# Kernel tuning notes

Measured on AMD Instinct MI355X. Metric: run time of the kernel, lower is better.

Reference implementation:

```python
import jax, jax.numpy as jnp
import numpy as np
from jax import lax

TOP_K = 4
ROUTED_SCALING = 1.0
RENORMALIZE = True


def setup_inputs() -> dict:
    key = jax.random.key(0)
    ks = jax.random.split(key, 9)
    H, I, E = 2048, 1024, 16
    s = 0.02
    return {
        "hidden_states": jax.random.normal(ks[0], (2, 1024, H), jnp.float32),
        "gate_w": jax.random.normal(ks[1], (E, H), jnp.float32) * s,
        "expert_bias": jax.random.normal(ks[2], (E,), jnp.float32) * s,
        "w_gate": jax.random.normal(ks[3], (E, I, H), jnp.float32) * s,
        "w_up": jax.random.normal(ks[4], (E, I, H), jnp.float32) * s,
        "w_down": jax.random.normal(ks[5], (E, H, I), jnp.float32) * s,
        "sw_gate": jax.random.normal(ks[6], (I, H), jnp.float32) * s,
        "sw_up": jax.random.normal(ks[7], (I, H), jnp.float32) * s,
        "sw_down": jax.random.normal(ks[8], (H, I), jnp.float32) * s,
    }


def _swiglu_ffn(x, wg, wu, wd):
    # SiluAndMul(gate_up) -> down_proj
    return (jax.nn.silu(x @ wg.T) * (x @ wu.T)) @ wd.T


def reference(hidden_states, gate_w, expert_bias, w_gate, w_up, w_down,
              sw_gate, sw_up, sw_down):
    orig_shape = hidden_states.shape
    H = orig_shape[-1]
    x = hidden_states.reshape(-1, H)            # [T, H]
    T = x.shape[0]

    # --- sigmoid gating with score-correction bias (bias affects selection only) ---
    logits = x.astype(jnp.float32) @ gate_w.T    # [T, E] fp32 router
    scores = jax.nn.sigmoid(logits)
    _, topk_idx = lax.top_k(scores + expert_bias[None, :], TOP_K)   # [T, K]
    topk_w = jnp.take_along_axis(scores, topk_idx, axis=-1)         # raw scores
    if RENORMALIZE:
        topk_w = topk_w / jnp.sum(topk_w, axis=-1, keepdims=True)
    topk_w = topk_w * ROUTED_SCALING

    # scatter top-k weights into dense [T, E] combine matrix
    E = gate_w.shape[0]
    combine = jnp.zeros((T, E), dtype=x.dtype).at[
        jnp.arange(T)[:, None], topk_idx].set(topk_w.astype(x.dtype))

    # --- routed experts: scan over experts, weighted accumulate ---
    def step(acc, ws):
        wg, wu, wd, cw = ws                     # cw: [T] combine weights
        return acc + cw[:, None] * _swiglu_ffn(x, wg, wu, wd), None

    routed, _ = lax.scan(step, jnp.zeros_like(x),
                         (w_gate, w_up, w_down, combine.T))

    # --- shared expert ---
    shared = _swiglu_ffn(x, sw_gate, sw_up, sw_down)

    return (routed + shared).reshape(orig_shape)
```

## Files before the change

kernel.cpp:

```cpp
#include <hip/hip_runtime.h>
#include <hip/hip_bf16.h>
#include <cstdint>

#define TK 2048
#define HD 2048
#define ID 1024
#define NE 16
#define NG 17
#define TOPK 4
#define SLOTS (TK*TOPK)
#define ROWS_ALL (SLOTS+TK)
#define IH (ID*HD)
#define MAXT 64

typedef __attribute__((ext_vector_type(4))) float f32x4;
typedef __attribute__((ext_vector_type(16))) float f32x16;
typedef __attribute__((ext_vector_type(8))) short s16x8;
typedef unsigned short u16;
typedef unsigned long long u64;

__device__ __forceinline__ u16 f2bf(float f){
  union { float f; uint32_t u; } v; v.f = f;
  uint32_t r = v.u + 0x7fffu + ((v.u >> 16) & 1u);
  return (u16)(r >> 16);
}

#define GLD16(g, l) __builtin_amdgcn_global_load_lds( \
    (const __attribute__((address_space(1))) void*)(g), \
    (__attribute__((address_space(3))) void*)(l), 16, 0, 0)

__device__ __forceinline__ const s16x8* fragp(const u16* b, int row, int off){
  return (const s16x8*)((const char*)b + row*128 + (off ^ ((row&7)<<4)));
}

#define MFMA32(a,b,c) __builtin_amdgcn_mfma_f32_32x32x16_bf16((a),(b),(c),0,0,0)

__global__ void k_prep(const float* __restrict__ x, u16* __restrict__ xb,
                       u64* __restrict__ maskbits, int* __restrict__ tokcnt){
  int gi = blockIdx.x*blockDim.x + threadIdx.x;
  int st = gridDim.x*blockDim.x;
  if (gi < NE*32) maskbits[gi] = 0ull;
  if (gi < TK) tokcnt[gi] = 0;
  for (int i=gi; i<TK*HD/4; i+=st){
    float4 f = ((const float4*)x)[i];
    ushort4 o; o.x=f2bf(f.x); o.y=f2bf(f.y); o.z=f2bf(f.z); o.w=f2bf(f.w);
    ((ushort4*)xb)[i] = o;
  }
}

__global__ void k_cvtw(const float* __restrict__ wg, const float* __restrict__ wu,
                       const float* __restrict__ wd, const float* __restrict__ swg,
                       const float* __restrict__ swu, const float* __restrict__ swd,
                       u16* __restrict__ wgu, u16* __restrict__ wdb){
  const size_t ngu = (size_t)NG*2048*(HD/4);
  const size_t nd  = (size_t)NG*2048*(ID/4);
  for (size_t i = (size_t)blockIdx.x*blockDim.x + threadIdx.x; i < ngu + nd;
       i += (size_t)gridDim.x*blockDim.x){
    const float4* src; ushort4* dst;
    if (i < ngu){
      int g   = (int)(i / (2048*(size_t)(HD/4)));
      int rem = (int)(i % (2048*(size_t)(HD/4)));
      int J   = rem / (HD/4);
      int kv  = rem % (HD/4);
      int rp  = (J>>6)*32 + (J&31);
      const float* s;
      if (g < NE) s = ((J&32) ? wu : wg) + (size_t)g*IH + (size_t)rp*HD;
      else        s = ((J&32) ? swu : swg) + (size_t)rp*HD;
      src = (const float4*)s + kv;
      dst = (ushort4*)(wgu + (size_t)g*2048*HD + (size_t)J*HD) + kv;
    } else {
      size_t j = i - ngu;
      int g   = (int)(j / (2048*(size_t)(ID/4)));
      int rem = (int)(j % (2048*(size_t)(ID/4)));
      int J   = rem / (ID/4);
      int kv  = rem % (ID/4);
      const float* s = (g < NE) ? (wd + (size_t)g*IH + (size_t)J*ID)
                                : (swd + (size_t)J*ID);
      src = (const float4*)s + kv;
      dst = (ushort4*)(wdb + (size_t)g*2048*ID + (size_t)J*ID) + kv;
    }
    float4 f = *src;
    ushort4 o; o.x=f2bf(f.x); o.y=f2bf(f.y); o.z=f2bf(f.z); o.w=f2bf(f.w);
    *dst = o;
  }
}

__global__ __launch_bounds__(256) void k_logits(const float* __restrict__ x,
                                                const float* __restrict__ gw,
                                                const float* __restrict__ bias,
                                                float* __restrict__ wdense,
                                                u64* __restrict__ maskbits){
  int t = blockIdx.x, tid = threadIdx.x;
  int lane = tid & 63, wv = tid >> 6;
  const float* xr = x + (size_t)t*HD;
  float acc[NE];
  #pragma unroll
  for (int e=0;e<NE;e++) acc[e]=0.f;
  for (int k=tid;k<HD;k+=256){
    float xv = xr[k];
    #pragma unroll
    for (int e=0;e<NE;e++) acc[e] += xv * gw[e*HD + k];
  }
  __shared__ float red[NE][4];
  #pragma unroll
  for (int e=0;e<NE;e++){
    float v = acc[e];
    #pragma unroll
    for (int off=32;off>0;off>>=1) v += __shfl_down(v, off, 64);
    if (lane==0) red[e][wv] = v;
  }
  __syncthreads();
  if (tid == 0){
    float sc[NE], bs[NE];
    #pragma unroll
    for (int e=0;e<NE;e++){
      float l = red[e][0]+red[e][1]+red[e][2]+red[e][3];
      float s = 1.f/(1.f+expf(-l));
      sc[e]=s; bs[e]=s+bias[e];
    }
    int idx[TOPK]; float wsum=0.f; unsigned used=0;
    for (int k=0;k<TOPK;k++){
      int best=0; float bv=-1e30f;
      for (int e=0;e<NE;e++) if (!((used>>e)&1u) && bs[e] > bv){ bv=bs[e]; best=e; }
      used |= 1u<<best; idx[k]=best; wsum += sc[best];
    }
    float inv = 1.f/wsum;
    for (int k=0;k<TOPK;k++){
      int e = idx[k];
      wdense[t*NE + e] = sc[e]*inv;
      atomicOr(&maskbits[e*32 + (t>>6)], 1ull << (t&63));
    }
  }
}

__global__ void k_scan(const u64* __restrict__ maskbits, int* __restrict__ counts,
                       int* __restrict__ offsets, int* __restrict__ wordpfx,
                       int* __restrict__ tiles){
  int acc = 0;
  for (int e=0;e<NE;e++){
    int c = 0;
    for (int w=0;w<32;w++){ wordpfx[e*32+w] = c; c += __popcll(maskbits[e*32+w]); }
    counts[e] = c;
  }
  for (int e=0;e<NE;e++){ offsets[e] = acc; acc += counts[e]; }
  offsets[NE] = acc;
  counts[NE] = TK;
  int nt = 0;
  for (int g=0; g<NG; g++){
    int c = counts[g];
    for (int mt=0; mt*256 < c && nt < MAXT; mt++) tiles[nt++] = (g<<8) | mt;
  }
  for (; nt<MAXT; nt++) tiles[nt] = -1;
}

__global__ void k_scatter(const u64* __restrict__ maskbits, const int* __restrict__ offsets,
                          const int* __restrict__ wordpfx, const float* __restrict__ wdense,
                          int* __restrict__ rowtok, float* __restrict__ roww,
                          int* __restrict__ tokcnt, int* __restrict__ tok4){
  int t = blockIdx.x*blockDim.x + threadIdx.x;
  int e = blockIdx.y;
  if (t >= TK) return;
  if (e == NE){ rowtok[offsets[NE]+t] = t; roww[offsets[NE]+t] = 1.f; return; }
  u64 w = maskbits[e*32 + (t>>6)];
  if ((w >> (t&63)) & 1ull){
    int pos = offsets[e] + wordpfx[e*32 + (t>>6)] + __popcll(w & ((1ull << (t&63)) - 1ull));
    rowtok[pos] = t; roww[pos] = wdense[t*NE + e];
    int r = atomicAdd(&tokcnt[t], 1);
    tok4[t*TOPK + r] = pos;
  }
}

__global__ __launch_bounds__(512, 2) void k_gemm1b(
    const u16* __restrict__ xb, const u16* __restrict__ wgu,
    const int* __restrict__ counts, const int* __restrict__ offsets,
    const int* __restrict__ rowtok, const float* __restrict__ roww,
    const int* __restrict__ tiles, u16* __restrict__ P)
{
  int te = tiles[blockIdx.y];
  if (te < 0) return;
  int g = te >> 8, mt = te & 255;
  int cnt = counts[g];
  int x = blockIdx.x;
  int base = offsets[g];
  const u16* B0 = wgu + (size_t)g*2048*HD + (size_t)(x*256)*HD;

  __shared__ u16 lsA[2][256*64];
  __shared__ u16 lsB[2][256*64];

  int tid = threadIdx.x, lane = tid & 63, wv = tid >> 6;
  int wm = (wv>>2)*128, wc = wv & 3;
  int rl = lane & 31, hi = lane >> 5;

  f32x16 acc[4][2] = {};

  const u16 *aSrc[4], *bSrc[4];
  #pragma unroll
  for (int i=0;i<4;i++){
    int c = i*512 + tid, r = c>>3, cb = c&7;
    int m = mt*256 + r; if (m >= cnt) m = cnt-1;
    int tok = rowtok[base + m];
    aSrc[i] = xb + (size_t)tok*HD + ((cb ^ (r&7))<<3);
    bSrc[i] = B0 + (size_t)r*HD + ((cb ^ (r&7))<<3);
  }

  #pragma unroll
  for (int i=0;i<4;i++) GLD16(aSrc[i], &lsA[0][(i*512 + wv*64)*8]);
  #pragma unroll
  for (int i=0;i<4;i++) GLD16(bSrc[i], &lsB[0][(i*512 + wv*64)*8]);

  const int ntile = HD/64;
  for (int t=0; t<ntile; ++t){
    int cur = t & 1, nxt = cur ^ 1;
    if (t+1 < ntile){
      int k1 = (t+1)*64;
      #pragma unroll
      for (int i=0;i<4;i++) GLD16(aSrc[i]+k1, &lsA[nxt][(i*512 + wv*64)*8]);
      #pragma unroll
      for (int i=0;i<4;i++) GLD16(bSrc[i]+k1, &lsB[nxt][(i*512 + wv*64)*8]);
      asm volatile("s_waitcnt vmcnt(8)" ::: "memory");
    } else {
      asm volatile("s_waitcnt vmcnt(0)" ::: "memory");
    }
    __builtin_amdgcn_s_barrier();
    const u16* A = lsA[cur]; const u16* B = lsB[cur];
    __builtin_amdgcn_s_setprio(1);
    #pragma unroll
    for (int s=0; s<4; ++s){
      int off = s*32 + hi*16;
      s16x8 af[4], bf[2];
      #pragma unroll
      for (int mi=0;mi<4;mi++) af[mi] = *fragp(A, wm + mi*32 + rl, off);
      bf[0] = *fragp(B, wc*64 + rl, off);
      bf[1] = *fragp(B, wc*64 + 32 + rl, off);
      #pragma unroll
      for (int mi=0;mi<4;mi++){
        acc[mi][0] = MFMA32(af[mi], bf[0], acc[mi][0]);
        acc[mi][1] = MFMA32(af[mi], bf[1], acc[mi][1]);
      }
    }
    __builtin_amdgcn_s_setprio(0);
    asm volatile("s_waitcnt lgkmcnt(0)" ::: "memory");
    __builtin_amdgcn_s_barrier();
  }
  int pcol = x*128 + wc*32 + rl;
  #pragma unroll
  for (int mi=0;mi<4;mi++){
    #pragma unroll
    for (int r=0;r<16;r++){
      int rowb = wm + mi*32 + (r&3) + 8*(r>>2) + 4*hi;
      int m = mt*256 + rowb;
      if (m < cnt){
        int slot = base + m;
        float wgt = roww[slot];
        float gv = acc[mi][0][r], uv = acc[mi][1][r];
        float pv = gv/(1.f+expf(-gv))*uv*wgt;
        P[(size_t)slot*ID + pcol] = f2bf(pv);
      }
    }
  }
}

__global__ __launch_bounds__(512, 2) void k_gemm2b(
    const u16* __restrict__ P, const u16* __restrict__ wdb,
    const int* __restrict__ counts, const int* __restrict__ offsets,
    const int* __restrict__ tiles, u16* __restrict__ R)
{
  int te = tiles[blockIdx.y];
  if (te < 0) return;
  int g = te >> 8, mt = te & 255;
  int cnt = counts[g];
  int base = offsets[g];
  int x = blockIdx.x;
  const u16* B0 = wdb + (size_t)g*2048*ID + (size_t)(x*256)*ID;

  __shared__ u16 lsA[2][256*64];
  __shared__ u16 lsB[2][256*64];

  int tid = threadIdx.x, lane = tid & 63, wv = tid >> 6;
  int wm = (wv>>2)*128, wc = wv & 3;
  int rl = lane & 31, hi = lane >> 5;
  f32x16 acc[4][2] = {};

  const u16 *aSrc[4], *bSrc[4];
  #pragma unroll
  for (int i=0;i<4;i++){
    int c = i*512 + tid, r = c>>3, cb = c&7;
    int m = mt*256 + r; if (m >= cnt) m = cnt-1;
    aSrc[i] = P + (size_t)(base + m)*ID + ((cb ^ (r&7))<<3);
    bSrc[i] = B0 + (size_t)r*ID + ((cb ^ (r&7))<<3);
  }

  #pragma unroll
  for (int i=0;i<4;i++) GLD16(aSrc[i], &lsA[0][(i*512 + wv*64)*8]);
  #pragma unroll
  for (int i=0;i<4;i++) GLD16(bSrc[i], &lsB[0][(i*512 + wv*64)*8]);

  const int ntile = ID/64;
  for (int t=0; t<ntile; ++t){
    int cur = t & 1, nxt = cur ^ 1;
    if (t+1 < ntile){
      int k1 = (t+1)*64;
      #pragma unroll
      for (int i=0;i<4;i++) GLD16(aSrc[i]+k1, &lsA[nxt][(i*512 + wv*64)*8]);
      #pragma unroll
      for (int i=0;i<4;i++) GLD16(bSrc[i]+k1, &lsB[nxt][(i*512 + wv*64)*8]);
      asm volatile("s_waitcnt vmcnt(8)" ::: "memory");
    } else {
      asm volatile("s_waitcnt vmcnt(0)" ::: "memory");
    }
    __builtin_amdgcn_s_barrier();
    const u16* A = lsA[cur]; const u16* B = lsB[cur];
    __builtin_amdgcn_s_setprio(1);
    #pragma unroll
    for (int s=0; s<4; ++s){
      int off = s*32 + hi*16;
      s16x8 af[4], bf[2];
      #pragma unroll
      for (int mi=0;mi<4;mi++) af[mi] = *fragp(A, wm + mi*32 + rl, off);
      bf[0] = *fragp(B, wc*64 + rl, off);
      bf[1] = *fragp(B, wc*64 + 32 + rl, off);
      #pragma unroll
      for (int mi=0;mi<4;mi++){
        acc[mi][0] = MFMA32(af[mi], bf[0], acc[mi][0]);
        acc[mi][1] = MFMA32(af[mi], bf[1], acc[mi][1]);
      }
    }
    __builtin_amdgcn_s_setprio(0);
    asm volatile("s_waitcnt lgkmcnt(0)" ::: "memory");
    __builtin_amdgcn_s_barrier();
  }
  #pragma unroll
  for (int mi=0;mi<4;mi++){
    #pragma unroll
    for (int r=0;r<16;r++){
      int rowb = wm + mi*32 + (r&3) + 8*(r>>2) + 4*hi;
      int m = mt*256 + rowb;
      if (m < cnt){
        int slot = base + m;
        u16* rrow = R + (size_t)slot*HD + x*256 + wc*64 + rl;
        rrow[0]  = f2bf(acc[mi][0][r]);
        rrow[32] = f2bf(acc[mi][1][r]);
      }
    }
  }
}

__global__ __launch_bounds__(256) void k_reduce(const u16* __restrict__ R,
                                                const int* __restrict__ tok4,
                                                float* __restrict__ out){
  int t = blockIdx.x;
  int c0 = threadIdx.x * 8;
  int s0 = tok4[t*TOPK+0], s1 = tok4[t*TOPK+1], s2 = tok4[t*TOPK+2], s3 = tok4[t*TOPK+3];
  const ushort4* p0 = (const ushort4*)(R + (size_t)s0*HD + c0);
  const ushort4* p1 = (const ushort4*)(R + (size_t)s1*HD + c0);
  const ushort4* p2 = (const ushort4*)(R + (size_t)s2*HD + c0);
  const ushort4* p3 = (const ushort4*)(R + (size_t)s3*HD + c0);
  const ushort4* ps = (const ushort4*)(R + (size_t)(SLOTS + t)*HD + c0);
  float* o = out + (size_t)t*HD + c0;
  #pragma unroll
  for (int h=0; h<2; h++){
    ushort4 a = p0[h], b = p1[h], c = p2[h], d = p3[h], e = ps[h];
    #pragma unroll
    for (int j=0;j<4;j++){
      u16 ua = ((const u16*)&a)[j], ub = ((const u16*)&b)[j];
      u16 uc = ((const u16*)&c)[j], ud = ((const u16*)&d)[j], ue = ((const u16*)&e)[j];
      union { uint32_t u; float f; } w;
      float v;
      w.u = (uint32_t)ua<<16; v  = w.f;
      w.u = (uint32_t)ub<<16; v += w.f;
      w.u = (uint32_t)uc<<16; v += w.f;
      w.u = (uint32_t)ud<<16; v += w.f;
      w.u = (uint32_t)ue<<16; v += w.f;
      o[h*4 + j] = v;
    }
  }
}


extern "C" void kernel_launch(void* const* d_in, const int* in_sizes, int n_in,
                              void* d_out, int out_size, void* d_ws, size_t ws_size,
                              hipStream_t stream){
  (void)in_sizes; (void)n_in; (void)ws_size; (void)out_size;
  const float* x       = (const float*)d_in[0];
  const float* gate_w  = (const float*)d_in[1];
  const float* ebias   = (const float*)d_in[2];
  const float* w_gate  = (const float*)d_in[3];
  const float* w_up    = (const float*)d_in[4];
  const float* w_down  = (const float*)d_in[5];
  const float* sw_gate = (const float*)d_in[6];
  const float* sw_up   = (const float*)d_in[7];
  const float* sw_down = (const float*)d_in[8];
  float* out = (float*)d_out;

  char* p = (char*)d_ws;
  auto alloc = [&](size_t bytes)->char*{ char* r = p; p += (bytes + 255) & ~(size_t)255; return r; };
  u16*   xb       = (u16*)  alloc((size_t)TK*HD*2);
  u16*   P        = (u16*)  alloc((size_t)ROWS_ALL*ID*2);
  float* wdense   = (float*)alloc((size_t)TK*NE*4);
  u64*   maskbits = (u64*)  alloc((size_t)NE*32*8);
  int*   wordpfx  = (int*)  alloc((size_t)NE*32*4);
  int*   counts   = (int*)  alloc(64);
  int*   offsets  = (int*)  alloc(64);
  int*   tiles    = (int*)  alloc(MAXT*4);
  int*   rowtok   = (int*)  alloc((size_t)ROWS_ALL*4);
  float* roww     = (float*)alloc((size_t)ROWS_ALL*4);
  int*   tokcnt   = (int*)  alloc((size_t)TK*4);
  int*   tok4     = (int*)  alloc((size_t)TK*TOPK*4);
  u16* wgu = (u16*)alloc((size_t)NG*2048*HD*2);
  u16* wdb = (u16*)alloc((size_t)NG*2048*ID*2);
  u16* R = wgu;

  k_prep<<<2048, 256, 0, stream>>>(x, xb, maskbits, tokcnt);
  k_cvtw<<<2048, 256, 0, stream>>>(w_gate, w_up, w_down, sw_gate, sw_up, sw_down,
                                   wgu, wdb);
  k_logits<<<TK, 256, 0, stream>>>(x, gate_w, ebias, wdense, maskbits);
  k_scan<<<1, 1, 0, stream>>>(maskbits, counts, offsets, wordpfx, tiles);
  k_scatter<<<dim3(TK/256, NG), 256, 0, stream>>>(maskbits, offsets, wordpfx, wdense,
                                                  rowtok, roww, tokcnt, tok4);

  dim3 g1(ID/128, MAXT);
  k_gemm1b<<<g1, 512, 0, stream>>>(xb, wgu, counts, offsets, rowtok, roww, tiles, P);
  dim3 g2(HD/256, MAXT);
  k_gemm2b<<<g2, 512, 0, stream>>>(P, wdb, counts, offsets, tiles, R);
  k_reduce<<<TK, 256, 0, stream>>>(R, tok4, out);
}
```

Baseline: 422.8 us.

## Restructure expert GEMMs into 16x16x32 MFMA with split-K interleaved staging

Both grouped expert GEMM kernels now use the 16x16x32 bf16 MFMA instead of 32x32x16. Each 64-wide K tile is split into two 32-wide halves held in separate LDS sub-buffers, with a 4-wide XOR swizzle. Each K step is broken into four compute phases that issue the next tile's A/B half-loads between MFMA bursts, guarded by finer vmcnt waits. The goal is to overlap global-to-LDS traffic with matrix math more evenly instead of issuing all prefetches at once. In exchange there are roughly four times as many barriers per K step and more fragment reads, and the epilogue mapping is rewritten to match the new accumulator layout.

```diff
diff --git a/kernel.cpp b/kernel.cpp
--- a/kernel.cpp
+++ b/kernel.cpp
@@ -14,7 +14,6 @@
 #define MAXT 64
 
 typedef __attribute__((ext_vector_type(4))) float f32x4;
-typedef __attribute__((ext_vector_type(16))) float f32x16;
 typedef __attribute__((ext_vector_type(8))) short s16x8;
 typedef unsigned short u16;
 typedef unsigned long long u64;
@@ -29,11 +28,7 @@
     (const __attribute__((address_space(1))) void*)(g), \
     (__attribute__((address_space(3))) void*)(l), 16, 0, 0)
 
-__device__ __forceinline__ const s16x8* fragp(const u16* b, int row, int off){
-  return (const s16x8*)((const char*)b + row*128 + (off ^ ((row&7)<<4)));
-}
-
-#define MFMA32(a,b,c) __builtin_amdgcn_mfma_f32_32x32x16_bf16((a),(b),(c),0,0,0)
+#define MFMA16(a,b,c) __builtin_amdgcn_mfma_f32_16x16x32_bf16((a),(b),(c),0,0,0)
 
 __global__ void k_prep(const float* __restrict__ x, u16* __restrict__ xb,
                        u64* __restrict__ maskbits, int* __restrict__ tokcnt){
@@ -184,77 +179,136 @@
   int base = offsets[g];
   const u16* B0 = wgu + (size_t)g*2048*HD + (size_t)(x*256)*HD;
 
-  __shared__ u16 lsA[2][256*64];
-  __shared__ u16 lsB[2][256*64];
+  __shared__ u16 lsA[2][2][256*32];
+  __shared__ u16 lsB[2][2][256*32];
 
   int tid = threadIdx.x, lane = tid & 63, wv = tid >> 6;
-  int wm = (wv>>2)*128, wc = wv & 3;
-  int rl = lane & 31, hi = lane >> 5;
-
-  f32x16 acc[4][2] = {};
-
-  const u16 *aSrc[4], *bSrc[4];
-  #pragma unroll
-  for (int i=0;i<4;i++){
-    int c = i*512 + tid, r = c>>3, cb = c&7;
+  int wm = (wv>>2)*128, wc = wv & 3, wn = wc*64;
+  int rl = lane & 15, hi = lane >> 4;
+
+  f32x4 acc[8][4] = {};
+
+  const u16 *aS[2], *bS[2];
+  #pragma unroll
+  for (int i=0;i<2;i++){
+    int c = i*512 + tid, r = c>>2, cb = c&3;
     int m = mt*256 + r; if (m >= cnt) m = cnt-1;
-    int tok = rowtok[base + m];
-    aSrc[i] = xb + (size_t)tok*HD + ((cb ^ (r&7))<<3);
-    bSrc[i] = B0 + (size_t)r*HD + ((cb ^ (r&7))<<3);
-  }
-
-  #pragma unroll
-  for (int i=0;i<4;i++) GLD16(aSrc[i], &lsA[0][(i*512 + wv*64)*8]);
-  #pragma unroll
-  for (int i=0;i<4;i++) GLD16(bSrc[i], &lsB[0][(i*512 + wv*64)*8]);
-
-  const int ntile = HD/64;
-  for (int t=0; t<ntile; ++t){
-    int cur = t & 1, nxt = cur ^ 1;
-    if (t+1 < ntile){
-      int k1 = (t+1)*64;
-      #pragma unroll
-      for (int i=0;i<4;i++) GLD16(aSrc[i]+k1, &lsA[nxt][(i*512 + wv*64)*8]);
-      #pragma unroll
-      for (int i=0;i<4;i++) GLD16(bSrc[i]+k1, &lsB[nxt][(i*512 + wv*64)*8]);
-      asm volatile("s_waitcnt vmcnt(8)" ::: "memory");
-    } else {
-      asm volatile("s_waitcnt vmcnt(0)" ::: "memory");
-    }
-    __builtin_amdgcn_s_barrier();
-    const u16* A = lsA[cur]; const u16* B = lsB[cur];
-    __builtin_amdgcn_s_setprio(1);
-    #pragma unroll
-    for (int s=0; s<4; ++s){
-      int off = s*32 + hi*16;
-      s16x8 af[4], bf[2];
-      #pragma unroll
-      for (int mi=0;mi<4;mi++) af[mi] = *fragp(A, wm + mi*32 + rl, off);
-      bf[0] = *fragp(B, wc*64 + rl, off);
-      bf[1] = *fragp(B, wc*64 + 32 + rl, off);
-      #pragma unroll
-      for (int mi=0;mi<4;mi++){
-        acc[mi][0] = MFMA32(af[mi], bf[0], acc[mi][0]);
-        acc[mi][1] = MFMA32(af[mi], bf[1], acc[mi][1]);
-      }
-    }
-    __builtin_amdgcn_s_setprio(0);
-    asm volatile("s_waitcnt lgkmcnt(0)" ::: "memory");
-    __builtin_amdgcn_s_barrier();
-  }
-  int pcol = x*128 + wc*32 + rl;
-  #pragma unroll
-  for (int mi=0;mi<4;mi++){
-    #pragma unroll
-    for (int r=0;r<16;r++){
-      int rowb = wm + mi*32 + (r&3) + 8*(r>>2) + 4*hi;
-      int m = mt*256 + rowb;
+    aS[i] = xb + (size_t)rowtok[base+m]*HD + ((cb ^ (r&3))<<3);
+    bS[i] = B0 + (size_t)r*HD + ((cb ^ (r&3))<<3);
+  }
+  auto stageA = [&](int buf, int s, int kb){
+    #pragma unroll
+    for (int i=0;i<2;i++) GLD16(aS[i] + kb + s*32, &lsA[buf][s][(i*512 + wv*64)*8]);
+  };
+  auto stageB = [&](int buf, int s, int kb){
+    #pragma unroll
+    for (int i=0;i<2;i++) GLD16(bS[i] + kb + s*32, &lsB[buf][s][(i*512 + wv*64)*8]);
+  };
+  auto rdA = [&](int buf, int s, int row)->s16x8{
+    return *(const s16x8*)((const char*)&lsA[buf][s][0] + row*64 + ((hi*16) ^ ((row&3)<<4)));
+  };
+  auto rdB = [&](int buf, int s, int row)->s16x8{
+    return *(const s16x8*)((const char*)&lsB[buf][s][0] + row*64 + ((hi*16) ^ ((row&3)<<4)));
+  };
+
+  stageA(0,0,0); stageB(0,0,0); stageA(0,1,0); stageB(0,1,0);
+  asm volatile("s_waitcnt vmcnt(4)" ::: "memory");
+  __builtin_amdgcn_s_barrier();
+
+  const int NT = HD/64;
+  for (int kt=0; kt<NT; ++kt){
+    int cur = kt & 1, nxt = cur ^ 1;
+    bool more = (kt+1 < NT);
+    int kn = (kt+1)*64;
+    s16x8 bf0[4], bf1[4];
+    {
+      s16x8 af[4];
+      #pragma unroll
+      for (int nj=0;nj<4;nj++) bf0[nj] = rdB(cur,0, wn + nj*16 + rl);
+      #pragma unroll
+      for (int mi=0;mi<4;mi++) af[mi] = rdA(cur,0, wm + mi*16 + rl);
+      if (more) stageA(nxt, 0, kn);
+      __builtin_amdgcn_s_barrier();
+      asm volatile("s_waitcnt lgkmcnt(0)" ::: "memory");
+      __builtin_amdgcn_s_setprio(1);
+      #pragma unroll
+      for (int mi=0;mi<4;mi++)
+        #pragma unroll
+        for (int nj=0;nj<4;nj++)
+          acc[mi][nj] = MFMA16(af[mi], bf0[nj], acc[mi][nj]);
+      __builtin_amdgcn_s_setprio(0);
+      __builtin_amdgcn_s_barrier();
+    }
+    {
+      s16x8 af[4];
+      #pragma unroll
+      for (int mi=0;mi<4;mi++) af[mi] = rdA(cur,0, wm + 64 + mi*16 + rl);
+      if (more) stageB(nxt, 0, kn);
+      __builtin_amdgcn_s_barrier();
+      asm volatile("s_waitcnt lgkmcnt(0)" ::: "memory");
+      __builtin_amdgcn_s_setprio(1);
+      #pragma unroll
+      for (int mi=0;mi<4;mi++)
+        #pragma unroll
+        for (int nj=0;nj<4;nj++)
+          acc[4+mi][nj] = MFMA16(af[mi], bf0[nj], acc[4+mi][nj]);
+      __builtin_amdgcn_s_setprio(0);
+      if (more) asm volatile("s_waitcnt vmcnt(4)" ::: "memory");
+      else      asm volatile("s_waitcnt vmcnt(0)" ::: "memory");
+      __builtin_amdgcn_s_barrier();
+    }
+    {
+      s16x8 af[4];
+      #pragma unroll
+      for (int nj=0;nj<4;nj++) bf1[nj] = rdB(cur,1, wn + nj*16 + rl);
+      #pragma unroll
+      for (int mi=0;mi<4;mi++) af[mi] = rdA(cur,1, wm + mi*16 + rl);
+      if (more) stageA(nxt, 1, kn);
+      __builtin_amdgcn_s_barrier();
+      asm volatile("s_waitcnt lgkmcnt(0)" ::: "memory");
+      __builtin_amdgcn_s_setprio(1);
+      #pragma unroll
+      for (int mi=0;mi<4;mi++)
+        #pragma unroll
+        for (int nj=0;nj<4;nj++)
+          acc[mi][nj] = MFMA16(af[mi], bf1[nj], acc[mi][nj]);
+      __builtin_amdgcn_s_setprio(0);
+      __builtin_amdgcn_s_barrier();
+    }
+    {
+      s16x8 af[4];
+      #pragma unroll
+      for (int mi=0;mi<4;mi++) af[mi] = rdA(cur,1, wm + 64 + mi*16 + rl);
+      if (more) stageB(nxt, 1, kn);
+      __builtin_amdgcn_s_barrier();
+      asm volatile("s_waitcnt lgkmcnt(0)" ::: "memory");
+      __builtin_amdgcn_s_setprio(1);
+      #pragma unroll
+      for (int mi=0;mi<4;mi++)
+        #pragma unroll
+        for (int nj=0;nj<4;nj++)
+          acc[4+mi][nj] = MFMA16(af[mi], bf1[nj], acc[4+mi][nj]);
+      __builtin_amdgcn_s_setprio(0);
+      if (more) asm volatile("s_waitcnt vmcnt(4)" ::: "memory");
+      __builtin_amdgcn_s_barrier();
+    }
+  }
+  #pragma unroll
+  for (int am=0; am<8; am++){
+    int msub = am>>2, mi = am&3;
+    #pragma unroll
+    for (int j=0;j<4;j++){
+      int m = mt*256 + wm + msub*64 + mi*16 + hi*4 + j;
       if (m < cnt){
         int slot = base + m;
         float wgt = roww[slot];
-        float gv = acc[mi][0][r], uv = acc[mi][1][r];
-        float pv = gv/(1.f+expf(-gv))*uv*wgt;
-        P[(size_t)slot*ID + pcol] = f2bf(pv);
+        #pragma unroll
+        for (int nj=0;nj<2;nj++){
+          float gv = acc[am][nj][j], uv = acc[am][nj+2][j];
+          float pv = gv/(1.f+expf(-gv))*uv*wgt;
+          int gcol = (x*4 + wc)*32 + nj*16 + rl;
+          P[(size_t)slot*ID + gcol] = f2bf(pv);
+        }
       }
     }
   }
@@ -273,73 +327,131 @@
   int x = blockIdx.x;
   const u16* B0 = wdb + (size_t)g*2048*ID + (size_t)(x*256)*ID;
 
-  __shared__ u16 lsA[2][256*64];
-  __shared__ u16 lsB[2][256*64];
+  __shared__ u16 lsA[2][2][256*32];
+  __shared__ u16 lsB[2][2][256*32];
 
   int tid = threadIdx.x, lane = tid & 63, wv = tid >> 6;
-  int wm = (wv>>2)*128, wc = wv & 3;
-  int rl = lane & 31, hi = lane >> 5;
-  f32x16 acc[4][2] = {};
-
-  const u16 *aSrc[4], *bSrc[4];
-  #pragma unroll
-  for (int i=0;i<4;i++){
-    int c = i*512 + tid, r = c>>3, cb = c&7;
+  int wm = (wv>>2)*128, wc = wv & 3, wn = wc*64;
+  int rl = lane & 15, hi = lane >> 4;
+
+  f32x4 acc[8][4] = {};
+
+  const u16 *aS[2], *bS[2];
+  #pragma unroll
+  for (int i=0;i<2;i++){
+    int c = i*512 + tid, r = c>>2, cb = c&3;
     int m = mt*256 + r; if (m >= cnt) m = cnt-1;
-    aSrc[i] = P + (size_t)(base + m)*ID + ((cb ^ (r&7))<<3);
-    bSrc[i] = B0 + (size_t)r*ID + ((cb ^ (r&7))<<3);
-  }
-
-  #pragma unroll
-  for (int i=0;i<4;i++) GLD16(aSrc[i], &lsA[0][(i*512 + wv*64)*8]);
-  #pragma unroll
-  for (int i=0;i<4;i++) GLD16(bSrc[i], &lsB[0][(i*512 + wv*64)*8]);
-
-  const int ntile = ID/64;
-  for (int t=0; t<ntile; ++t){
-    int cur = t & 1, nxt = cur ^ 1;
-    if (t+1 < ntile){
-      int k1 = (t+1)*64;
-      #pragma unroll
-      for (int i=0;i<4;i++) GLD16(aSrc[i]+k1, &lsA[nxt][(i*512 + wv*64)*8]);
-      #pragma unroll
-      for (int i=0;i<4;i++) GLD16(bSrc[i]+k1, &lsB[nxt][(i*512 + wv*64)*8]);
-      asm volatile("s_waitcnt vmcnt(8)" ::: "memory");
-    } else {
-      asm volatile("s_waitcnt vmcnt(0)" ::: "memory");
-    }
-    __builtin_amdgcn_s_barrier();
-    const u16* A = lsA[cur]; const u16* B = lsB[cur];
-    __builtin_amdgcn_s_setprio(1);
-    #pragma unroll
-    for (int s=0; s<4; ++s){
-      int off = s*32 + hi*16;
-      s16x8 af[4], bf[2];
-      #pragma unroll
-      for (int mi=0;mi<4;mi++) af[mi] = *fragp(A, wm + mi*32 + rl, off);
-      bf[0] = *fragp(B, wc*64 + rl, off);
-      bf[1] = *fragp(B, wc*64 + 32 + rl, off);
-      #pragma unroll
-      for (int mi=0;mi<4;mi++){
-        acc[mi][0] = MFMA32(af[mi], bf[0], acc[mi][0]);
-        acc[mi][1] = MFMA32(af[mi], bf[1], acc[mi][1]);
-      }
-    }
-    __builtin_amdgcn_s_setprio(0);
-    asm volatile("s_waitcnt lgkmcnt(0)" ::: "memory");
-    __builtin_amdgcn_s_barrier();
-  }
-  #pragma unroll
-  for (int mi=0;mi<4;mi++){
-    #pragma unroll
-    for (int r=0;r<16;r++){
-      int rowb = wm + mi*32 + (r&3) + 8*(r>>2) + 4*hi;
-      int m = mt*256 + rowb;
+    aS[i] = P  + (size_t)(base + m)*ID + ((cb ^ (r&3))<<3);
+    bS[i] = B0 + (size_t)r*ID + ((cb ^ (r&3))<<3);
+  }
+  auto stageA = [&](int buf, int s, int kb){
+    #pragma unroll
+    for (int i=0;i<2;i++) GLD16(aS[i] + kb + s*32, &lsA[buf][s][(i*512 + wv*64)*8]);
+  };
+  auto stageB = [&](int buf, int s, int kb){
+    #pragma unroll
+    for (int i=0;i<2;i++) GLD16(bS[i] + kb + s*32, &lsB[buf][s][(i*512 + wv*64)*8]);
+  };
+  auto rdA = [&](int buf, int s, int row)->s16x8{
+    return *(const s16x8*)((const char*)&lsA[buf][s][0] + row*64 + ((hi*16) ^ ((row&3)<<4)));
+  };
+  auto rdB = [&](int buf, int s, int row)->s16x8{
+    return *(const s16x8*)((const char*)&lsB[buf][s][0] + row*64 + ((hi*16) ^ ((row&3)<<4)));
+  };
+
+  stageA(0,0,0); stageB(0,0,0); stageA(0,1,0); stageB(0,1,0);
+  asm volatile("s_waitcnt vmcnt(4)" ::: "memory");
+  __builtin_amdgcn_s_barrier();
+
+  const int NT = ID/64;
+  for (int kt=0; kt<NT; ++kt){
+    int cur = kt & 1, nxt = cur ^ 1;
+    bool more = (kt+1 < NT);
+    int kn = (kt+1)*64;
+    s16x8 bf0[4], bf1[4];
+    {
+      s16x8 af[4];
+      #pragma unroll
+      for (int nj=0;nj<4;nj++) bf0[nj] = rdB(cur,0, wn + nj*16 + rl);
+      #pragma unroll
+      for (int mi=0;mi<4;mi++) af[mi] = rdA(cur,0, wm + mi*16 + rl);
+      if (more) stageA(nxt, 0, kn);
+      __builtin_amdgcn_s_barrier();
+      asm volatile("s_waitcnt lgkmcnt(0)" ::: "memory");
+      __builtin_amdgcn_s_setprio(1);
+      #pragma unroll
+      for (int mi=0;mi<4;mi++)
+        #pragma unroll
+        for (int nj=0;nj<4;nj++)
+          acc[mi][nj] = MFMA16(af[mi], bf0[nj], acc[mi][nj]);
+      __builtin_amdgcn_s_setprio(0);
+      __builtin_amdgcn_s_barrier();
+    }
+    {
+      s16x8 af[4];
+      #pragma unroll
+      for (int mi=0;mi<4;mi++) af[mi] = rdA(cur,0, wm + 64 + mi*16 + rl);
+      if (more) stageB(nxt, 0, kn);
+      __builtin_amdgcn_s_barrier();
+      asm volatile("s_waitcnt lgkmcnt(0)" ::: "memory");
+      __builtin_amdgcn_s_setprio(1);
+      #pragma unroll
+      for (int mi=0;mi<4;mi++)
+        #pragma unroll
+        for (int nj=0;nj<4;nj++)
+          acc[4+mi][nj] = MFMA16(af[mi], bf0[nj], acc[4+mi][nj]);
+      __builtin_amdgcn_s_setprio(0);
+      if (more) asm volatile("s_waitcnt vmcnt(4)" ::: "memory");
+      else      asm volatile("s_waitcnt vmcnt(0)" ::: "memory");
+      __builtin_amdgcn_s_barrier();
+    }
+    {
+      s16x8 af[4];
+      #pragma unroll
+      for (int nj=0;nj<4;nj++) bf1[nj] = rdB(cur,1, wn + nj*16 + rl);
+      #pragma unroll
+      for (int mi=0;mi<4;mi++) af[mi] = rdA(cur,1, wm + mi*16 + rl);
+      if (more) stageA(nxt, 1, kn);
+      __builtin_amdgcn_s_barrier();
+      asm volatile("s_waitcnt lgkmcnt(0)" ::: "memory");
+      __builtin_amdgcn_s_setprio(1);
+      #pragma unroll
+      for (int mi=0;mi<4;mi++)
+        #pragma unroll
+        for (int nj=0;nj<4;nj++)
+          acc[mi][nj] = MFMA16(af[mi], bf1[nj], acc[mi][nj]);
+      __builtin_amdgcn_s_setprio(0);
+      __builtin_amdgcn_s_barrier();
+    }
+    {
+      s16x8 af[4];
+      #pragma unroll
+      for (int mi=0;mi<4;mi++) af[mi] = rdA(cur,1, wm + 64 + mi*16 + rl);
+      if (more) stageB(nxt, 1, kn);
+      __builtin_amdgcn_s_barrier();
+      asm volatile("s_waitcnt lgkmcnt(0)" ::: "memory");
+      __builtin_amdgcn_s_setprio(1);
+      #pragma unroll
+      for (int mi=0;mi<4;mi++)
+        #pragma unroll
+        for (int nj=0;nj<4;nj++)
+          acc[4+mi][nj] = MFMA16(af[mi], bf1[nj], acc[4+mi][nj]);
+      __builtin_amdgcn_s_setprio(0);
+      if (more) asm volatile("s_waitcnt vmcnt(4)" ::: "memory");
+      __builtin_amdgcn_s_barrier();
+    }
+  }
+  #pragma unroll
+  for (int am=0; am<8; am++){
+    int msub = am>>2, mi = am&3;
+    #pragma unroll
+    for (int j=0;j<4;j++){
+      int m = mt*256 + wm + msub*64 + mi*16 + hi*4 + j;
       if (m < cnt){
         int slot = base + m;
-        u16* rrow = R + (size_t)slot*HD + x*256 + wc*64 + rl;
-        rrow[0]  = f2bf(acc[mi][0][r]);
-        rrow[32] = f2bf(acc[mi][1][r]);
+        u16* rrow = R + (size_t)slot*HD + x*256 + wn + rl;
+        #pragma unroll
+        for (int nj=0;nj<4;nj++) rrow[nj*16] = f2bf(acc[am][nj][j]);
       }
     }
   }
```

Result: slower. 452.5 us (+7.0%).
